# Kernel optimization log

Hardware: AMD Instinct MI355X
Metric: run time of the kernel (lower is better)

The kernel has to match this reference:

```python
import jax, jax.numpy as jnp
import numpy as np
import math

D_MODEL = 1024
N_HEAD = 16
D_HEAD = D_MODEL // N_HEAD
INIT_SIZE = 1200  # RelativeSinusoidalPositionalEmbedding init_size
SCALE = 1.0       # scale=False in __init__


def _rel_pos_embed(L, d_head):
    """Replicates RelativeSinusoidalPositionalEmbedding: table over positions
    [-601, 600] (num=init_size+1=1201 rows), padding row 0 zeroed, then gather
    rows for positions arange(-L/2, L/2) + origin_shift (origin_shift=601)."""
    num = INIT_SIZE + 1                      # 1201
    half = d_head // 2
    freq = jnp.exp(jnp.arange(half, dtype=jnp.float32) * (-math.log(10000.0) / (half - 1)))
    pos_vals = jnp.arange(-num // 2, num // 2, dtype=jnp.float32)   # -601..599 -> 1201 vals
    ang = pos_vals[:, None] * freq[None, :]
    table = jnp.concatenate([jnp.sin(ang), jnp.cos(ang)], axis=1)   # [num, d_head]
    table = table.at[0].set(0.0)             # padding_idx = 0
    origin_shift = num // 2 + 1              # 601
    idx = jnp.arange(-(L // 2), L // 2) + origin_shift   # L even -> L indices
    return table[idx]                        # [L, d_head]


def setup_inputs() -> dict:
    key = jax.random.key(0)
    k1, k2, k3, k4, k5 = jax.random.split(key, 5)
    B, L = 4, 1024
    embed = jax.random.normal(k1, (B, L, D_MODEL), dtype=jnp.float32)
    umask = jnp.ones((B, L), dtype=jnp.int32)                       # 1 = valid utterance
    qmask = jax.random.randint(k2, (B, L), 0, 2).astype(jnp.int64)  # speaker ids {0,1}
    W_qkv = jax.random.normal(k3, (D_MODEL, 4 * D_MODEL), dtype=jnp.float32) * 0.02
    W_pos = jax.random.normal(k4, (D_HEAD, 3 * D_MODEL), dtype=jnp.float32) * 0.02
    W_fc  = jax.random.normal(k5, (D_MODEL, D_MODEL), dtype=jnp.float32) * 0.02
    return {"embed": embed, "umask": umask, "qmask": qmask,
            "W_qkv": W_qkv, "W_pos": W_pos, "W_fc": W_fc}


def reference(embed, umask, qmask, W_qkv, W_pos, W_fc):
    B, L, d = embed.shape
    H, dh = N_HEAD, d // N_HEAD

    # qkv projection and head split
    q, k1, k2, v = jnp.split(embed @ W_qkv, 4, axis=-1)             # each [B, L, d]
    q  = q.reshape(B, L, H, dh).transpose(0, 2, 1, 3)               # [B, H, L, dh]
    k1 = k1.reshape(B, L, H, dh).transpose(0, 2, 1, 3)
    k2 = k2.reshape(B, L, H, dh).transpose(0, 2, 1, 3)
    v  = v.reshape(B, L, H, dh).transpose(0, 2, 1, 3)

    # relative position projections (detached sinusoids -> qk_pos linear)
    pe = _rel_pos_embed(L, dh)                                      # [L, dh]
    qp, kp1, kp2 = jnp.split(pe @ W_pos, 3, axis=-1)                # each [L, d]
    qp  = qp.reshape(L, H, dh).transpose(1, 0, 2)                   # [H, L, dh]
    kp1 = kp1.reshape(L, H, dh).transpose(1, 0, 2)
    kp2 = kp2.reshape(L, H, dh).transpose(1, 0, 2)

    pos1 = jnp.einsum('hqd,hkd->hqk', qp, kp1)                      # [H, L, L]
    pos2 = jnp.einsum('hqd,hkd->hqk', qp, kp2)

    attn_self  = jnp.einsum('bhqd,bhkd->bhqk', q, k1) + pos1[None]  # [B, H, L, L]
    attn_other = jnp.einsum('bhqd,bhkd->bhqk', q, k2) + pos2[None]

    # same-speaker mask: self-attn only where speakers match, other-attn where they differ
    qeq = (qmask[:, :, None] == qmask[:, None, :])                  # [B, L, L] bool
    attn_self  = jnp.where(qeq[:, None], attn_self, 0.0)
    attn_other = jnp.where(qeq[:, None], 0.0, attn_other)
    attn_add = (attn_self + attn_other) / SCALE

    # causal (order) mask + padding mask (eval-mode path of the module)
    order = jnp.triu(jnp.ones((L, L), dtype=bool), 1)[None] | (umask == 0)[:, None, :]
    attn = jnp.where(order[:, None], -jnp.inf, attn_add)
    p = jax.nn.softmax(attn, axis=-1)                               # dropout is identity in eval

    out = jnp.einsum('bhqk,bhkd->bhqd', p, v)                       # [B, H, L, dh]
    out = out.transpose(0, 2, 1, 3).reshape(B, L, d)
    return out @ W_fc
```

## Files before the change

### kernel.cpp

```cpp
#include <hip/hip_runtime.h>
#include <math.h>

#define NB 4
#define SEQ 1024
#define DMODEL 1024
#define NHEAD 16
#define DHEAD 64

typedef __attribute__((ext_vector_type(8))) short s16x8;
typedef __attribute__((ext_vector_type(4))) short s16x4;
typedef __attribute__((ext_vector_type(4))) float f32x4;

__device__ __forceinline__ short f2bf(float f) {
    union { float f; unsigned u; } x; x.f = f;
    unsigned r = x.u + 0x7fffu + ((x.u >> 16) & 1u);
    return (short)(r >> 16);
}

__device__ __forceinline__ unsigned cvtpk(float lo, float hi) {
    unsigned r;
    asm("v_cvt_pk_bf16_f32 %0, %1, %2" : "=v"(r) : "v"(lo), "v"(hi));
    return r;
}

__device__ __forceinline__ f32x4 mfma16(s16x8 a, s16x8 b, f32x4 c) {
    return __builtin_amdgcn_mfma_f32_16x16x32_bf16(a, b, c, 0, 0, 0);
}

__device__ __forceinline__ s16x8 cvt8(float4 a, float4 b) {
    s16x8 v;
    v[0] = f2bf(a.x); v[1] = f2bf(a.y); v[2] = f2bf(a.z); v[3] = f2bf(a.w);
    v[4] = f2bf(b.x); v[5] = f2bf(b.y); v[6] = f2bf(b.z); v[7] = f2bf(b.w);
    return v;
}

__device__ __forceinline__ s16x8 ldlds(const short* base, int byteoff) {
    return *(const s16x8*)((const char*)base + byteoff);
}

#define GLDS16(g, l) __builtin_amdgcn_global_load_lds( \
    (const __attribute__((address_space(1))) unsigned int*)(g), \
    (__attribute__((address_space(3))) unsigned int*)(l), 16, 0, 0)
#define GLDS4(g, l) __builtin_amdgcn_global_load_lds( \
    (const __attribute__((address_space(1))) unsigned int*)(g), \
    (__attribute__((address_space(3))) unsigned int*)(l), 4, 0, 0)

__global__ __launch_bounds__(256) void prep_kernel(
    const int* __restrict__ qmask, const int* __restrict__ umask,
    const float* __restrict__ Wpos, const float* __restrict__ embed,
    const float* __restrict__ Wqkv, const float* __restrict__ Wfc,
    int* __restrict__ PM, short* __restrict__ qpb,
    short* __restrict__ k1cat, short* __restrict__ k2cat,
    short* __restrict__ ebf, short* __restrict__ WqkvT,
    short* __restrict__ WfcT)
{
    __shared__ __align__(16) char smem[9216];
    int gbid = blockIdx.x;
    int tid = threadIdx.x;

    if (gbid < 4) {
        int b = gbid;
        for (int k = tid; k < 1088; k += 256) {
            int v = 2;
            if (k < 1024)
                v = (qmask[b * 1024 + k] & 1) | ((umask[b * 1024 + k] == 0) ? 2 : 0);
            PM[b * 1088 + k] = v;
        }
    } else if (gbid < 388) {
        int bid = gbid - 4;
        int s = bid >> 7;
        int l0 = (bid & 127) * 8;
        float (*pe)[64] = (float(*)[64])smem;

        for (int idx = tid; idx < 512; idx += 256) {
            int li = idx >> 6, t = idx & 63;
            float p = (float)(l0 + li - 512);
            int j = (t < 32) ? t : (t - 32);
            float f = expf(-0.2971077539f * (float)j);
            float a = p * f;
            pe[li][t] = (t < 32) ? sinf(a) : cosf(a);
        }
        __syncthreads();

        float acc[4][8] = {};
        const float* wp = Wpos + s * 1024 + tid;
        for (int t = 0; t < 64; ++t) {
            float w0 = wp[t * 3072];
            float w1 = wp[t * 3072 + 256];
            float w2 = wp[t * 3072 + 512];
            float w3 = wp[t * 3072 + 768];
            #pragma unroll
            for (int li = 0; li < 8; ++li) {
                float pv = pe[li][t];
                acc[0][li] += pv * w0; acc[1][li] += pv * w1;
                acc[2][li] += pv * w2; acc[3][li] += pv * w3;
            }
        }
        #pragma unroll
        for (int cc = 0; cc < 4; ++cc) {
            int c = tid + cc * 256;
            int h = c >> 6, d = c & 63;
            #pragma unroll
            for (int li = 0; li < 8; ++li) {
                short bv = f2bf(acc[cc][li]);
                if (s == 0) {
                    qpb[((size_t)(h << 10) + l0 + li) * 64 + d] = bv;
                } else {
                    short* dst = (s == 1) ? k1cat : k2cat;
                    #pragma unroll
                    for (int bb = 0; bb < 4; ++bb)
                        dst[((size_t)((bb * 16 + h) * 1024) + l0 + li) * 128 + 64 + d] = bv;
                }
            }
        }
    } else if (gbid < 2436) {
        int i = ((gbid - 388) * 256 + tid) * 8;
        float4 a = *(const float4*)(embed + i);
        float4 b = *(const float4*)(embed + i + 4);
        *(s16x8*)(ebf + i) = cvt8(a, b);
    } else {
        const float* W; short* WT; int N, bx, by;
        if (gbid < 3460) {
            int t = gbid - 2436;
            W = Wqkv; WT = WqkvT; N = 4096;
            bx = t & 63; by = t >> 6;
        } else {
            int t = gbid - 3460;
            W = Wfc; WT = WfcT; N = 1024;
            bx = t & 15; by = t >> 4;
        }
        short (*T)[72] = (short(*)[72])smem;
        int nt = bx * 64, kt = by * 64;
        int kl = tid >> 4;
        int nl = (tid & 15) * 4;
        #pragma unroll
        for (int rr = 0; rr < 4; ++rr) {
            int k = kl + rr * 16;
            float4 v = *(const float4*)(W + (size_t)(kt + k) * N + nt + nl);
            T[nl + 0][k] = f2bf(v.x);
            T[nl + 1][k] = f2bf(v.y);
            T[nl + 2][k] = f2bf(v.z);
            T[nl + 3][k] = f2bf(v.w);
        }
        __syncthreads();
        int nr = tid >> 2;
        int kc = (tid & 3) * 16;
        uint4 a = *(const uint4*)&T[nr][kc];
        uint4 b = *(const uint4*)&T[nr][kc + 8];
        short* dst = WT + (size_t)(nt + nr) * 1024 + kt + kc;
        *(uint4*)(dst) = a;
        *(uint4*)(dst + 8) = b;
    }
}

template<int EPI, int NCOLS>
__global__ __launch_bounds__(256) void gemm_nt(
    const short* __restrict__ A, const short* __restrict__ BT,
    short* __restrict__ o0, short* __restrict__ o1, short* __restrict__ o2,
    short* __restrict__ o3, float* __restrict__ of)
{
    __shared__ short As[128 * 32];
    __shared__ short Bs[128 * 32];

    int nwg = gridDim.x * gridDim.y;
    int lin = blockIdx.y * gridDim.x + blockIdx.x;
    int cpx = nwg >> 3;
    int swb = (lin & 7) * cpx + (lin >> 3);
    int bx = swb % gridDim.x, by = swb / gridDim.x;
    int m0 = by * 128, n0 = bx * 128;

    int tid = threadIdx.x;
    int w = tid >> 6, lane = tid & 63;
    int wm = w >> 1, wn = w & 1;
    int lq = lane & 15, lg = lane >> 4;

    f32x4 zero = {0.f, 0.f, 0.f, 0.f};
    f32x4 acc[4][4];
    #pragma unroll
    for (int i = 0; i < 4; ++i)
        #pragma unroll
        for (int j = 0; j < 4; ++j) acc[i][j] = zero;

    int swz = (((lane & 3) ^ ((lane >> 2) & 3)) << 3);
    int srow = lane >> 2;
    const short* aBase = A  + (size_t)(m0 + (w << 5) + srow) * 1024 + swz;
    const short* bBase = BT + (size_t)(n0 + (w << 5) + srow) * 1024 + swz;
    short* aDst = As + w * 1024;
    short* bDst = Bs + w * 1024;

    for (int kt = 0; kt < 1024; kt += 32) {
        __syncthreads();
        GLDS16(aBase + kt, aDst);
        GLDS16(aBase + kt + 16 * 1024, aDst + 512);
        GLDS16(bBase + kt, bDst);
        GLDS16(bBase + kt + 16 * 1024, bDst + 512);
        __syncthreads();

        s16x8 af[4], bfr[4];
        #pragma unroll
        for (int mt = 0; mt < 4; ++mt) {
            int row = wm * 64 + mt * 16 + lq;
            af[mt] = ldlds(As, (row * 64 + lg * 16) ^ ((row & 3) << 4));
        }
        #pragma unroll
        for (int nt = 0; nt < 4; ++nt) {
            int row = wn * 64 + nt * 16 + lq;
            bfr[nt] = ldlds(Bs, (row * 64 + lg * 16) ^ ((row & 3) << 4));
        }
        #pragma unroll
        for (int mt = 0; mt < 4; ++mt)
            #pragma unroll
            for (int nt = 0; nt < 4; ++nt)
                acc[mt][nt] = mfma16(af[mt], bfr[nt], acc[mt][nt]);
    }

    #pragma unroll
    for (int nt = 0; nt < 4; ++nt) {
        int n = n0 + wn * 64 + nt * 16 + lq;
        int sec = n >> 10, hd = n & 1023;
        int hh = hd >> 6, d = hd & 63;
        #pragma unroll
        for (int mt = 0; mt < 4; ++mt) {
            int mb = m0 + wm * 64 + mt * 16 + lg * 4;
            if constexpr (EPI == 1) {
                #pragma unroll
                for (int r = 0; r < 4; ++r)
                    of[(size_t)(mb + r) * NCOLS + n] = acc[mt][nt][r];
            } else {
                int b = mb >> 10, li0 = mb & 1023;
                int bh = b * 16 + hh;
                if (sec == 3) {
                    s16x4 pv;
                    #pragma unroll
                    for (int r = 0; r < 4; ++r) pv[r] = f2bf(acc[mt][nt][r]);
                    *(s16x4*)(o3 + (((size_t)(bh * 64 + d)) << 10) + li0) = pv;
                } else {
                    #pragma unroll
                    for (int r = 0; r < 4; ++r) {
                        short bv = f2bf(acc[mt][nt][r]);
                        if (sec == 0)
                            o0[((size_t)(bh << 10) + li0 + r) * 64 + d] = bv;
                        else if (sec == 1)
                            o1[((size_t)bh * 1024 + li0 + r) * 128 + d] = bv;
                        else
                            o2[((size_t)bh * 1024 + li0 + r) * 128 + d] = bv;
                    }
                }
            }
        }
    }
}

__global__ __launch_bounds__(256) void attn_kernel(
    const short* __restrict__ qb, const short* __restrict__ k1cat,
    const short* __restrict__ k2cat, const short* __restrict__ vtb,
    const short* __restrict__ qpb, const int* __restrict__ PM,
    const int* __restrict__ qmask, short* __restrict__ ctx)
{
    __shared__ short K1s[2][32 * 128];
    __shared__ short K2s[2][32 * 128];
    __shared__ short Vs[2][64 * 32];
    __shared__ int   PMs[2][64];

    int bid = blockIdx.x;
    int xg = bid & 7, jj = bid >> 3;
    int bh = xg * 8 + (jj & 7);
    int pair = jj >> 3;
    int b = bh >> 4, h = bh & 15;

    int w = threadIdx.x >> 6, lane = threadIdx.x & 63;
    int lq = lane & 15, lg = lane >> 4;

    auto STAGE = [&](int d, int K0) {
        #pragma unroll
        for (int i = 0; i < 5; ++i) {
            int g = w * 5 + i;
            if (g < 8) {
                int row = g * 4 + (lane >> 4);
                int colb = ((lane & 15) << 4) ^ ((row & 7) << 4);
                const short* src = k1cat + ((size_t)bh * 1024 + K0 + row) * 128 + (colb >> 1);
                GLDS16(src, &K1s[d][g * 512]);
            } else if (g < 16) {
                int gg = g - 8;
                int row = gg * 4 + (lane >> 4);
                int colb = ((lane & 15) << 4) ^ ((row & 7) << 4);
                const short* src = k2cat + ((size_t)bh * 1024 + K0 + row) * 128 + (colb >> 1);
                GLDS16(src, &K2s[d][gg * 512]);
            } else {
                int c = g - 16;
                int row = c * 16 + (lane >> 2);
                int colb = ((lane & 3) << 4) ^ ((row & 3) << 4);
                const short* src = vtb + ((size_t)bh * 64 + row) * 1024 + K0 + (colb >> 1);
                GLDS16(src, &Vs[d][c * 512]);
            }
        }
        if (w == 0) {
            GLDS4(PM + b * 1088 + K0 + lane, &PMs[d][0]);
        }
    };

    f32x4 zero = {0.f, 0.f, 0.f, 0.f};

    #pragma unroll 1
    for (int phase = 0; phase < 2; ++phase) {
        int qt = phase ? (15 - pair) : pair;
        int q0 = qt * 64 + w * 16;
        int q_glob = q0 + lq;

        const short* qrow  = qb  + ((size_t)bh * SEQ + q_glob) * DHEAD;
        const short* qprow = qpb + ((size_t)h  * SEQ + q_glob) * DHEAD;
        s16x8 qf0  = *(const s16x8*)(qrow + lg * 8);
        s16x8 qf1  = *(const s16x8*)(qrow + 32 + lg * 8);
        s16x8 qpf0 = *(const s16x8*)(qprow + lg * 8);
        s16x8 qpf1 = *(const s16x8*)(qprow + 32 + lg * 8);
        int qm_q = qmask[b * SEQ + q_glob] & 1;
        asm volatile("s_waitcnt vmcnt(0)" ::: "memory");

        f32x4 accO[4];
        #pragma unroll
        for (int i = 0; i < 4; ++i) accO[i] = zero;
        float m_run = -1e30f, l_run = 0.f;

        int nslab = 2 * qt + 2;
        STAGE(0, 0);

        #pragma unroll 1
        for (int t = 0; t < nslab; ++t) {
            int cur = t & 1;
            if (t + 1 < nslab) {
                STAGE(cur ^ 1, (t + 1) * 32);
                if (w == 0) asm volatile("s_waitcnt vmcnt(6)" ::: "memory");
                else        asm volatile("s_waitcnt vmcnt(5)" ::: "memory");
            } else {
                asm volatile("s_waitcnt vmcnt(0)" ::: "memory");
            }
            __builtin_amdgcn_s_barrier();
            asm volatile("" ::: "memory");

            int K0 = t * 32;
            if (K0 <= q0 + 15) {
                const short* b1 = K1s[cur];
                const short* b2 = K2s[cur];

                f32x4 s1v[2], s2v[2];
                __builtin_amdgcn_s_setprio(1);
                #pragma unroll
                for (int hh = 0; hh < 2; ++hh) {
                    int row = hh * 16 + lq;
                    int ro = row * 256 + (lg << 4);
                    int sw = (row & 7) << 4;
                    f32x4 tv = zero, uv = zero;
                    tv = mfma16(ldlds(b1, (ro      ) ^ sw), qf0,  tv);
                    tv = mfma16(ldlds(b1, (ro +  64) ^ sw), qf1,  tv);
                    tv = mfma16(ldlds(b1, (ro + 128) ^ sw), qpf0, tv);
                    tv = mfma16(ldlds(b1, (ro + 192) ^ sw), qpf1, tv);
                    s1v[hh] = tv;
                    uv = mfma16(ldlds(b2, (ro      ) ^ sw), qf0,  uv);
                    uv = mfma16(ldlds(b2, (ro +  64) ^ sw), qf1,  uv);
                    uv = mfma16(ldlds(b2, (ro + 128) ^ sw), qpf0, uv);
                    uv = mfma16(ldlds(b2, (ro + 192) ^ sw), qpf1, uv);
                    s2v[hh] = uv;
                }
                __builtin_amdgcn_s_setprio(0);

                int4 pmv0 = *(const int4*)&PMs[cur][lg * 4];
                int4 pmv1 = *(const int4*)&PMs[cur][16 + lg * 4];
                int pme[8] = {pmv0.x, pmv0.y, pmv0.z, pmv0.w,
                              pmv1.x, pmv1.y, pmv1.z, pmv1.w};

                float sv[8];
                #pragma unroll
                for (int i = 0; i < 8; ++i) {
                    int hh = i >> 2, r = i & 3;
                    int k_idx = K0 + hh * 16 + lg * 4 + r;
                    int pm = pme[i];
                    float s = ((pm & 1) == qm_q) ? s1v[hh][r] : s2v[hh][r];
                    if (k_idx > q_glob || (pm & 2)) s = -INFINITY;
                    sv[i] = s;
                }
                float tm = sv[0];
                #pragma unroll
                for (int i = 1; i < 8; ++i) tm = fmaxf(tm, sv[i]);
                tm = fmaxf(tm, __shfl_xor(tm, 16));
                tm = fmaxf(tm, __shfl_xor(tm, 32));

                if (!__all(tm <= m_run + 8.0f)) {
                    float m_new = fmaxf(m_run, tm);
                    float scale = __expf(m_run - m_new);
                    m_run = m_new;
                    l_run *= scale;
                    f32x4 scv;
                    scv[0] = __shfl(scale, lg * 4 + 0);
                    scv[1] = __shfl(scale, lg * 4 + 1);
                    scv[2] = __shfl(scale, lg * 4 + 2);
                    scv[3] = __shfl(scale, lg * 4 + 3);
                    #pragma unroll
                    for (int dt = 0; dt < 4; ++dt) accO[dt] *= scv;
                }

                float p[8]; float ps = 0.f;
                #pragma unroll
                for (int i = 0; i < 8; ++i) { p[i] = __expf(sv[i] - m_run); ps += p[i]; }
                ps += __shfl_xor(ps, 16);
                ps += __shfl_xor(ps, 32);
                l_run += ps;

                unsigned dA0 = cvtpk(p[0], p[1]);
                unsigned dA1 = cvtpk(p[2], p[3]);
                unsigned dB0 = cvtpk(p[4], p[5]);
                unsigned dB1 = cvtpk(p[6], p[7]);
                int sl0 = lq + ((lg & 1) << 5);
                int sl1 = sl0 + 16;
                unsigned a0 = (unsigned)__shfl((int)dA0, sl0), a1 = (unsigned)__shfl((int)dA1, sl0);
                unsigned a2 = (unsigned)__shfl((int)dA0, sl1), a3 = (unsigned)__shfl((int)dA1, sl1);
                unsigned c0 = (unsigned)__shfl((int)dB0, sl0), c1 = (unsigned)__shfl((int)dB1, sl0);
                unsigned c2 = (unsigned)__shfl((int)dB0, sl1), c3 = (unsigned)__shfl((int)dB1, sl1);
                bool hi = (lg >= 2);
                union { unsigned u[4]; s16x8 v; } pa;
                pa.u[0] = hi ? c0 : a0; pa.u[1] = hi ? c1 : a1;
                pa.u[2] = hi ? c2 : a2; pa.u[3] = hi ? c3 : a3;

                __builtin_amdgcn_s_setprio(1);
                #pragma unroll
                for (int dt = 0; dt < 4; ++dt) {
                    int vrow = dt * 16 + lq;
                    int voff = (vrow * 64 + (lg << 4)) ^ ((vrow & 3) << 4);
                    accO[dt] = mfma16(pa.v, ldlds(Vs[cur], voff), accO[dt]);
                }
                __builtin_amdgcn_s_setprio(0);
            }

            asm volatile("" ::: "memory");
            __builtin_amdgcn_s_barrier();
        }

        float inv = 1.0f / l_run;
        f32x4 invv;
        invv[0] = __shfl(inv, lg * 4 + 0);
        invv[1] = __shfl(inv, lg * 4 + 1);
        invv[2] = __shfl(inv, lg * 4 + 2);
        invv[3] = __shfl(inv, lg * 4 + 3);
        #pragma unroll
        for (int dt = 0; dt < 4; ++dt) {
            #pragma unroll
            for (int r = 0; r < 4; ++r) {
                int qo = q0 + lg * 4 + r;
                size_t off = ((size_t)(b * SEQ + qo)) * DMODEL + h * DHEAD + dt * 16 + lq;
                ctx[off] = f2bf(accO[dt][r] * invv[r]);
            }
        }
    }
}

extern "C" void kernel_launch(void* const* d_in, const int* in_sizes, int n_in,
                              void* d_out, int out_size, void* d_ws, size_t ws_size,
                              hipStream_t stream) {
    const float* embed = (const float*)d_in[0];
    const int*   umask = (const int*)d_in[1];
    const int*   qmask = (const int*)d_in[2];
    const float* Wqkv  = (const float*)d_in[3];
    const float* Wpos  = (const float*)d_in[4];
    const float* Wfc   = (const float*)d_in[5];
    float* out = (float*)d_out;

    char* w = (char*)d_ws;
    short* qb    = (short*)(w + (0ull  << 20));
    short* vtb   = (short*)(w + (8ull  << 20));
    short* qpb   = (short*)(w + (16ull << 20));
    short* ctx   = (short*)(w + (18ull << 20));
    short* ebf   = ctx;
    short* k1cat = (short*)(w + (26ull << 20));
    short* k2cat = (short*)(w + (42ull << 20));
    int*   PM    = (int*)  (w + (58ull << 20));
    short* WqkvT = (short*)(w + (59ull << 20));
    short* WfcT  = (short*)(w + (67ull << 20));

    hipLaunchKernelGGL(prep_kernel, dim3(3716), dim3(256), 0, stream,
                       qmask, umask, Wpos, embed, Wqkv, Wfc,
                       PM, qpb, k1cat, k2cat, ebf, WqkvT, WfcT);
    hipLaunchKernelGGL((gemm_nt<0, 4096>), dim3(32, 32), dim3(256), 0, stream,
                       ebf, WqkvT, qb, k1cat, k2cat, vtb, (float*)nullptr);
    hipLaunchKernelGGL(attn_kernel, dim3(512), dim3(256), 0, stream,
                       qb, k1cat, k2cat, vtb, qpb, PM, qmask, ctx);
    hipLaunchKernelGGL((gemm_nt<1, 1024>), dim3(8, 32), dim3(256), 0, stream,
                       ctx, WfcT, (short*)nullptr, (short*)nullptr, (short*)nullptr,
                       (short*)nullptr, out);
}
```

Baseline: 171.7 us.

## Double-buffer GEMM LDS tiles and split attention into one q-tile per block

The GEMM kernel now double-buffers its A/B shared-memory tiles, so the next K-slab's global-to-LDS loads are issued before the current slab's MFMAs and one barrier per iteration is dropped. The attention kernel no longer pairs two q-tiles (qt and 15-qt) per block. It launches 1024 blocks, each handling a single q-tile, ordered from heaviest to lightest to balance load. This aims to hide GEMM load latency and raise attention parallelism. In exchange the GEMM uses twice the LDS, which may lower occupancy, and attention pays per-block setup twice as often.

```diff
diff --git a/kernel.cpp b/kernel.cpp
--- a/kernel.cpp
+++ b/kernel.cpp
@@ -159,8 +159,8 @@
     short* __restrict__ o0, short* __restrict__ o1, short* __restrict__ o2,
     short* __restrict__ o3, float* __restrict__ of)
 {
-    __shared__ short As[128 * 32];
-    __shared__ short Bs[128 * 32];
+    __shared__ short As[2][128 * 32];
+    __shared__ short Bs[2][128 * 32];
 
     int nwg = gridDim.x * gridDim.y;
     int lin = blockIdx.y * gridDim.x + blockIdx.x;
@@ -185,33 +185,43 @@
     int srow = lane >> 2;
     const short* aBase = A  + (size_t)(m0 + (w << 5) + srow) * 1024 + swz;
     const short* bBase = BT + (size_t)(n0 + (w << 5) + srow) * 1024 + swz;
-    short* aDst = As + w * 1024;
-    short* bDst = Bs + w * 1024;
-
+    int dOff = w * 1024;
+
+    GLDS16(aBase, &As[0][dOff]);
+    GLDS16(aBase + 16 * 1024, &As[0][dOff + 512]);
+    GLDS16(bBase, &Bs[0][dOff]);
+    GLDS16(bBase + 16 * 1024, &Bs[0][dOff + 512]);
+    __syncthreads();
+
+    int cur = 0;
     for (int kt = 0; kt < 1024; kt += 32) {
-        __syncthreads();
-        GLDS16(aBase + kt, aDst);
-        GLDS16(aBase + kt + 16 * 1024, aDst + 512);
-        GLDS16(bBase + kt, bDst);
-        GLDS16(bBase + kt + 16 * 1024, bDst + 512);
-        __syncthreads();
+        if (kt + 32 < 1024) {
+            int nxt = cur ^ 1;
+            GLDS16(aBase + kt + 32, &As[nxt][dOff]);
+            GLDS16(aBase + kt + 32 + 16 * 1024, &As[nxt][dOff + 512]);
+            GLDS16(bBase + kt + 32, &Bs[nxt][dOff]);
+            GLDS16(bBase + kt + 32 + 16 * 1024, &Bs[nxt][dOff + 512]);
+        }
 
         s16x8 af[4], bfr[4];
         #pragma unroll
         for (int mt = 0; mt < 4; ++mt) {
             int row = wm * 64 + mt * 16 + lq;
-            af[mt] = ldlds(As, (row * 64 + lg * 16) ^ ((row & 3) << 4));
+            af[mt] = ldlds(As[cur], (row * 64 + lg * 16) ^ ((row & 3) << 4));
         }
         #pragma unroll
         for (int nt = 0; nt < 4; ++nt) {
             int row = wn * 64 + nt * 16 + lq;
-            bfr[nt] = ldlds(Bs, (row * 64 + lg * 16) ^ ((row & 3) << 4));
+            bfr[nt] = ldlds(Bs[cur], (row * 64 + lg * 16) ^ ((row & 3) << 4));
         }
         #pragma unroll
         for (int mt = 0; mt < 4; ++mt)
             #pragma unroll
             for (int nt = 0; nt < 4; ++nt)
                 acc[mt][nt] = mfma16(af[mt], bfr[nt], acc[mt][nt]);
+
+        __syncthreads();
+        cur ^= 1;
     }
 
     #pragma unroll
@@ -263,9 +273,9 @@
     __shared__ int   PMs[2][64];
 
     int bid = blockIdx.x;
-    int xg = bid & 7, jj = bid >> 3;
-    int bh = xg * 8 + (jj & 7);
-    int pair = jj >> 3;
+    int xg = bid & 7, j = bid >> 3;
+    int bh = xg * 8 + (j & 7);
+    int qt = 15 - (j >> 3);
     int b = bh >> 4, h = bh & 15;
 
     int w = threadIdx.x >> 6, lane = threadIdx.x & 63;
@@ -301,153 +311,149 @@
 
     f32x4 zero = {0.f, 0.f, 0.f, 0.f};
 
+    int q0 = qt * 64 + w * 16;
+    int q_glob = q0 + lq;
+
+    const short* qrow  = qb  + ((size_t)bh * SEQ + q_glob) * DHEAD;
+    const short* qprow = qpb + ((size_t)h  * SEQ + q_glob) * DHEAD;
+    s16x8 qf0  = *(const s16x8*)(qrow + lg * 8);
+    s16x8 qf1  = *(const s16x8*)(qrow + 32 + lg * 8);
+    s16x8 qpf0 = *(const s16x8*)(qprow + lg * 8);
+    s16x8 qpf1 = *(const s16x8*)(qprow + 32 + lg * 8);
+    int qm_q = qmask[b * SEQ + q_glob] & 1;
+    asm volatile("s_waitcnt vmcnt(0)" ::: "memory");
+
+    f32x4 accO[4];
+    #pragma unroll
+    for (int i = 0; i < 4; ++i) accO[i] = zero;
+    float m_run = -1e30f, l_run = 0.f;
+
+    int nslab = 2 * qt + 2;
+    STAGE(0, 0);
+
     #pragma unroll 1
-    for (int phase = 0; phase < 2; ++phase) {
-        int qt = phase ? (15 - pair) : pair;
-        int q0 = qt * 64 + w * 16;
-        int q_glob = q0 + lq;
-
-        const short* qrow  = qb  + ((size_t)bh * SEQ + q_glob) * DHEAD;
-        const short* qprow = qpb + ((size_t)h  * SEQ + q_glob) * DHEAD;
-        s16x8 qf0  = *(const s16x8*)(qrow + lg * 8);
-        s16x8 qf1  = *(const s16x8*)(qrow + 32 + lg * 8);
-        s16x8 qpf0 = *(const s16x8*)(qprow + lg * 8);
-        s16x8 qpf1 = *(const s16x8*)(qprow + 32 + lg * 8);
-        int qm_q = qmask[b * SEQ + q_glob] & 1;
-        asm volatile("s_waitcnt vmcnt(0)" ::: "memory");
-
-        f32x4 accO[4];
-        #pragma unroll
-        for (int i = 0; i < 4; ++i) accO[i] = zero;
-        float m_run = -1e30f, l_run = 0.f;
-
-        int nslab = 2 * qt + 2;
-        STAGE(0, 0);
-
-        #pragma unroll 1
-        for (int t = 0; t < nslab; ++t) {
-            int cur = t & 1;
-            if (t + 1 < nslab) {
-                STAGE(cur ^ 1, (t + 1) * 32);
-                if (w == 0) asm volatile("s_waitcnt vmcnt(6)" ::: "memory");
-                else        asm volatile("s_waitcnt vmcnt(5)" ::: "memory");
-            } else {
-                asm volatile("s_waitcnt vmcnt(0)" ::: "memory");
-            }
-            __builtin_amdgcn_s_barrier();
-            asm volatile("" ::: "memory");
-
-            int K0 = t * 32;
-            if (K0 <= q0 + 15) {
-                const short* b1 = K1s[cur];
-                const short* b2 = K2s[cur];
-
-                f32x4 s1v[2], s2v[2];
-                __builtin_amdgcn_s_setprio(1);
+    for (int t = 0; t < nslab; ++t) {
+        int cur = t & 1;
+        if (t + 1 < nslab) {
+            STAGE(cur ^ 1, (t + 1) * 32);
+            if (w == 0) asm volatile("s_waitcnt vmcnt(6)" ::: "memory");
+            else        asm volatile("s_waitcnt vmcnt(5)" ::: "memory");
+        } else {
+            asm volatile("s_waitcnt vmcnt(0)" ::: "memory");
+        }
+        __builtin_amdgcn_s_barrier();
+        asm volatile("" ::: "memory");
+
+        int K0 = t * 32;
+        if (K0 <= q0 + 15) {
+            const short* b1 = K1s[cur];
+            const short* b2 = K2s[cur];
+
+            f32x4 s1v[2], s2v[2];
+            __builtin_amdgcn_s_setprio(1);
+            #pragma unroll
+            for (int hh = 0; hh < 2; ++hh) {
+                int row = hh * 16 + lq;
+                int ro = row * 256 + (lg << 4);
+                int sw = (row & 7) << 4;
+                f32x4 tv = zero, uv = zero;
+                tv = mfma16(ldlds(b1, (ro      ) ^ sw), qf0,  tv);
+                tv = mfma16(ldlds(b1, (ro +  64) ^ sw), qf1,  tv);
+                tv = mfma16(ldlds(b1, (ro + 128) ^ sw), qpf0, tv);
+                tv = mfma16(ldlds(b1, (ro + 192) ^ sw), qpf1, tv);
+                s1v[hh] = tv;
+                uv = mfma16(ldlds(b2, (ro      ) ^ sw), qf0,  uv);
+                uv = mfma16(ldlds(b2, (ro +  64) ^ sw), qf1,  uv);
+                uv = mfma16(ldlds(b2, (ro + 128) ^ sw), qpf0, uv);
+                uv = mfma16(ldlds(b2, (ro + 192) ^ sw), qpf1, uv);
+                s2v[hh] = uv;
+            }
+            __builtin_amdgcn_s_setprio(0);
+
+            int4 pmv0 = *(const int4*)&PMs[cur][lg * 4];
+            int4 pmv1 = *(const int4*)&PMs[cur][16 + lg * 4];
+            int pme[8] = {pmv0.x, pmv0.y, pmv0.z, pmv0.w,
+                          pmv1.x, pmv1.y, pmv1.z, pmv1.w};
+
+            float sv[8];
+            #pragma unroll
+            for (int i = 0; i < 8; ++i) {
+                int hh = i >> 2, r = i & 3;
+                int k_idx = K0 + hh * 16 + lg * 4 + r;
+                int pm = pme[i];
+                float s = ((pm & 1) == qm_q) ? s1v[hh][r] : s2v[hh][r];
+                if (k_idx > q_glob || (pm & 2)) s = -INFINITY;
+                sv[i] = s;
+            }
+            float tm = sv[0];
+            #pragma unroll
+            for (int i = 1; i < 8; ++i) tm = fmaxf(tm, sv[i]);
+            tm = fmaxf(tm, __shfl_xor(tm, 16));
+            tm = fmaxf(tm, __shfl_xor(tm, 32));
+
+            if (!__all(tm <= m_run + 8.0f)) {
+                float m_new = fmaxf(m_run, tm);
+                float scale = __expf(m_run - m_new);
+                m_run = m_new;
+                l_run *= scale;
+                f32x4 scv;
+                scv[0] = __shfl(scale, lg * 4 + 0);
+                scv[1] = __shfl(scale, lg * 4 + 1);
+                scv[2] = __shfl(scale, lg * 4 + 2);
+                scv[3] = __shfl(scale, lg * 4 + 3);
                 #pragma unroll
-                for (int hh = 0; hh < 2; ++hh) {
-                    int row = hh * 16 + lq;
-                    int ro = row * 256 + (lg << 4);
-                    int sw = (row & 7) << 4;
-                    f32x4 tv = zero, uv = zero;
-                    tv = mfma16(ldlds(b1, (ro      ) ^ sw), qf0,  tv);
-                    tv = mfma16(ldlds(b1, (ro +  64) ^ sw), qf1,  tv);
-                    tv = mfma16(ldlds(b1, (ro + 128) ^ sw), qpf0, tv);
-                    tv = mfma16(ldlds(b1, (ro + 192) ^ sw), qpf1, tv);
-                    s1v[hh] = tv;
-                    uv = mfma16(ldlds(b2, (ro      ) ^ sw), qf0,  uv);
-                    uv = mfma16(ldlds(b2, (ro +  64) ^ sw), qf1,  uv);
-                    uv = mfma16(ldlds(b2, (ro + 128) ^ sw), qpf0, uv);
-                    uv = mfma16(ldlds(b2, (ro + 192) ^ sw), qpf1, uv);
-                    s2v[hh] = uv;
-                }
-                __builtin_amdgcn_s_setprio(0);
-
-                int4 pmv0 = *(const int4*)&PMs[cur][lg * 4];
-                int4 pmv1 = *(const int4*)&PMs[cur][16 + lg * 4];
-                int pme[8] = {pmv0.x, pmv0.y, pmv0.z, pmv0.w,
-                              pmv1.x, pmv1.y, pmv1.z, pmv1.w};
-
-                float sv[8];
-                #pragma unroll
-                for (int i = 0; i < 8; ++i) {
-                    int hh = i >> 2, r = i & 3;
-                    int k_idx = K0 + hh * 16 + lg * 4 + r;
-                    int pm = pme[i];
-                    float s = ((pm & 1) == qm_q) ? s1v[hh][r] : s2v[hh][r];
-                    if (k_idx > q_glob || (pm & 2)) s = -INFINITY;
-                    sv[i] = s;
-                }
-                float tm = sv[0];
-                #pragma unroll
-                for (int i = 1; i < 8; ++i) tm = fmaxf(tm, sv[i]);
-                tm = fmaxf(tm, __shfl_xor(tm, 16));
-                tm = fmaxf(tm, __shfl_xor(tm, 32));
-
-                if (!__all(tm <= m_run + 8.0f)) {
-                    float m_new = fmaxf(m_run, tm);
-                    float scale = __expf(m_run - m_new);
-                    m_run = m_new;
-                    l_run *= scale;
-                    f32x4 scv;
-                    scv[0] = __shfl(scale, lg * 4 + 0);
-                    scv[1] = __shfl(scale, lg * 4 + 1);
-                    scv[2] = __shfl(scale, lg * 4 + 2);
-                    scv[3] = __shfl(scale, lg * 4 + 3);
-                    #pragma unroll
-                    for (int dt = 0; dt < 4; ++dt) accO[dt] *= scv;
-                }
-
-                float p[8]; float ps = 0.f;
-                #pragma unroll
-                for (int i = 0; i < 8; ++i) { p[i] = __expf(sv[i] - m_run); ps += p[i]; }
-                ps += __shfl_xor(ps, 16);
-                ps += __shfl_xor(ps, 32);
-                l_run += ps;
-
-                unsigned dA0 = cvtpk(p[0], p[1]);
-                unsigned dA1 = cvtpk(p[2], p[3]);
-                unsigned dB0 = cvtpk(p[4], p[5]);
-                unsigned dB1 = cvtpk(p[6], p[7]);
-                int sl0 = lq + ((lg & 1) << 5);
-                int sl1 = sl0 + 16;
-                unsigned a0 = (unsigned)__shfl((int)dA0, sl0), a1 = (unsigned)__shfl((int)dA1, sl0);
-                unsigned a2 = (unsigned)__shfl((int)dA0, sl1), a3 = (unsigned)__shfl((int)dA1, sl1);
-                unsigned c0 = (unsigned)__shfl((int)dB0, sl0), c1 = (unsigned)__shfl((int)dB1, sl0);
-                unsigned c2 = (unsigned)__shfl((int)dB0, sl1), c3 = (unsigned)__shfl((int)dB1, sl1);
-                bool hi = (lg >= 2);
-                union { unsigned u[4]; s16x8 v; } pa;
-                pa.u[0] = hi ? c0 : a0; pa.u[1] = hi ? c1 : a1;
-                pa.u[2] = hi ? c2 : a2; pa.u[3] = hi ? c3 : a3;
-
-                __builtin_amdgcn_s_setprio(1);
-                #pragma unroll
-                for (int dt = 0; dt < 4; ++dt) {
-                    int vrow = dt * 16 + lq;
-                    int voff = (vrow * 64 + (lg << 4)) ^ ((vrow & 3) << 4);
-                    accO[dt] = mfma16(pa.v, ldlds(Vs[cur], voff), accO[dt]);
-                }
-                __builtin_amdgcn_s_setprio(0);
-            }
-
-            asm volatile("" ::: "memory");
-            __builtin_amdgcn_s_barrier();
-        }
-
-        float inv = 1.0f / l_run;
-        f32x4 invv;
-        invv[0] = __shfl(inv, lg * 4 + 0);
-        invv[1] = __shfl(inv, lg * 4 + 1);
-        invv[2] = __shfl(inv, lg * 4 + 2);
-        invv[3] = __shfl(inv, lg * 4 + 3);
-        #pragma unroll
-        for (int dt = 0; dt < 4; ++dt) {
-            #pragma unroll
-            for (int r = 0; r < 4; ++r) {
-                int qo = q0 + lg * 4 + r;
-                size_t off = ((size_t)(b * SEQ + qo)) * DMODEL + h * DHEAD + dt * 16 + lq;
-                ctx[off] = f2bf(accO[dt][r] * invv[r]);
-            }
+                for (int dt = 0; dt < 4; ++dt) accO[dt] *= scv;
+            }
+
+            float p[8]; float ps = 0.f;
+            #pragma unroll
+            for (int i = 0; i < 8; ++i) { p[i] = __expf(sv[i] - m_run); ps += p[i]; }
+            ps += __shfl_xor(ps, 16);
+            ps += __shfl_xor(ps, 32);
+            l_run += ps;
+
+            unsigned dA0 = cvtpk(p[0], p[1]);
+            unsigned dA1 = cvtpk(p[2], p[3]);
+            unsigned dB0 = cvtpk(p[4], p[5]);
+            unsigned dB1 = cvtpk(p[6], p[7]);
+            int sl0 = lq + ((lg & 1) << 5);
+            int sl1 = sl0 + 16;
+            unsigned a0 = (unsigned)__shfl((int)dA0, sl0), a1 = (unsigned)__shfl((int)dA1, sl0);
+            unsigned a2 = (unsigned)__shfl((int)dA0, sl1), a3 = (unsigned)__shfl((int)dA1, sl1);
+            unsigned c0 = (unsigned)__shfl((int)dB0, sl0), c1 = (unsigned)__shfl((int)dB1, sl0);
+            unsigned c2 = (unsigned)__shfl((int)dB0, sl1), c3 = (unsigned)__shfl((int)dB1, sl1);
+            bool hi = (lg >= 2);
+            union { unsigned u[4]; s16x8 v; } pa;
+            pa.u[0] = hi ? c0 : a0; pa.u[1] = hi ? c1 : a1;
+            pa.u[2] = hi ? c2 : a2; pa.u[3] = hi ? c3 : a3;
+
+            __builtin_amdgcn_s_setprio(1);
+            #pragma unroll
+            for (int dt = 0; dt < 4; ++dt) {
+                int vrow = dt * 16 + lq;
+                int voff = (vrow * 64 + (lg << 4)) ^ ((vrow & 3) << 4);
+                accO[dt] = mfma16(pa.v, ldlds(Vs[cur], voff), accO[dt]);
+            }
+            __builtin_amdgcn_s_setprio(0);
+        }
+
+        asm volatile("" ::: "memory");
+        __builtin_amdgcn_s_barrier();
+    }
+
+    float inv = 1.0f / l_run;
+    f32x4 invv;
+    invv[0] = __shfl(inv, lg * 4 + 0);
+    invv[1] = __shfl(inv, lg * 4 + 1);
+    invv[2] = __shfl(inv, lg * 4 + 2);
+    invv[3] = __shfl(inv, lg * 4 + 3);
+    #pragma unroll
+    for (int dt = 0; dt < 4; ++dt) {
+        #pragma unroll
+        for (int r = 0; r < 4; ++r) {
+            int qo = q0 + lg * 4 + r;
+            size_t off = ((size_t)(b * SEQ + qo)) * DMODEL + h * DHEAD + dt * 16 + lq;
+            ctx[off] = f2bf(accO[dt][r] * invv[r]);
         }
     }
 }
@@ -480,7 +486,7 @@
                        PM, qpb, k1cat, k2cat, ebf, WqkvT, WfcT);
     hipLaunchKernelGGL((gemm_nt<0, 4096>), dim3(32, 32), dim3(256), 0, stream,
                        ebf, WqkvT, qb, k1cat, k2cat, vtb, (float*)nullptr);
-    hipLaunchKernelGGL(attn_kernel, dim3(512), dim3(256), 0, stream,
+    hipLaunchKernelGGL(attn_kernel, dim3(1024), dim3(256), 0, stream,
                        qb, k1cat, k2cat, vtb, qpb, PM, qmask, ctx);
     hipLaunchKernelGGL((gemm_nt<1, 1024>), dim3(8, 32), dim3(256), 0, stream,
                        ctx, WfcT, (short*)nullptr, (short*)nullptr, (short*)nullptr,
```

Measured after the change: 167.6 us. 1.02x faster.
